# Kernel optimization log

Hardware: AMD Instinct MI355X
Metric: run time of the kernel (lower is better)

## Reference

```python
import jax, jax.numpy as jnp
import numpy as np

EPS = 216.0 / 24389.0
KAPPA = 24389.0 / 27.0
WP = jnp.array([0.95047, 1.0, 1.08883], dtype=jnp.float32)  # D65 white point
M_RGB2XYZ = jnp.array([[0.4124564, 0.3575761, 0.1804375],
                       [0.2126729, 0.7151522, 0.0721750],
                       [0.0193339, 0.1191920, 0.9503041]], dtype=jnp.float32)
M_XYZ2RGB = jnp.array([[3.2404542, -1.5371385, -0.4985314],
                       [-0.9692660, 1.8760108, 0.0415560],
                       [0.0556434, -0.2040259, 1.0572252]], dtype=jnp.float32)
GRID = 8          # cv2.createCLAHE tileGridSize=(8,8)
CLIP_LIMIT = 2.0  # cv2.createCLAHE clipLimit=2.0
NBINS = 256


def _srgb_to_linear(c):
    return jnp.where(c <= 0.04045, c / 12.92, ((c + 0.055) / 1.055) ** 2.4)


def _linear_to_srgb(c):
    c = jnp.maximum(c, 0.0)
    return jnp.where(c <= 0.0031308, c * 12.92, 1.055 * c ** (1.0 / 2.4) - 0.055)


def _rgb_to_lab(rgb):  # rgb [...,3] in [0,1]
    xyz = _srgb_to_linear(rgb) @ M_RGB2XYZ.T / WP
    f = jnp.where(xyz > EPS, jnp.cbrt(xyz), (KAPPA * xyz + 16.0) / 116.0)
    L = 116.0 * f[..., 1] - 16.0
    a = 500.0 * (f[..., 0] - f[..., 1])
    b = 200.0 * (f[..., 1] - f[..., 2])
    return L, a, b


def _lab_to_rgb(L, a, b):
    fy = (L + 16.0) / 116.0
    fx = fy + a / 500.0
    fz = fy - b / 200.0
    def finv(f):
        f3 = f ** 3
        return jnp.where(f3 > EPS, f3, (116.0 * f - 16.0) / KAPPA)
    xyz = jnp.stack([finv(fx), finv(fy), finv(fz)], axis=-1) * WP
    return jnp.clip(_linear_to_srgb(xyz @ M_XYZ2RGB.T), 0.0, 1.0)


def _quantize_L(L):  # cv2.normalize(..., 0, 255, NORM_MINMAX) per image + uint8 cast
    lmin = L.min(axis=(1, 2), keepdims=True)
    lmax = L.max(axis=(1, 2), keepdims=True)
    l255 = (L - lmin) / (lmax - lmin + 1e-6) * 255.0
    return jnp.clip(jnp.round(l255), 0, 255).astype(jnp.int32)


def _equalize_hist(l_int):  # cv2.equalizeHist per image, [N,H,W] int32 -> float levels
    N, H, W = l_int.shape
    seg = (jnp.arange(N, dtype=jnp.int32)[:, None, None] * NBINS + l_int).reshape(-1)
    hist = jax.ops.segment_sum(jnp.ones(seg.shape, jnp.float32), seg,
                               num_segments=N * NBINS).reshape(N, NBINS)
    lut = jnp.round(jnp.cumsum(hist, axis=1) * (255.0 / (H * W)))  # [N,256]
    return jnp.take_along_axis(lut, l_int.reshape(N, H * W), axis=1).reshape(N, H, W)


def _clahe(l_int):  # tiled clipped histogram equalization + bilinear LUT blend
    N, H, W = l_int.shape
    th, tw = H // GRID, W // GRID
    area = th * tw
    ty = jnp.arange(H, dtype=jnp.int32) // th
    tx = jnp.arange(W, dtype=jnp.int32) // tw
    tile = ty[:, None] * GRID + tx[None, :]                      # [H,W] tile id
    seg = ((jnp.arange(N, dtype=jnp.int32)[:, None, None] * (GRID * GRID) + tile)
           * NBINS + l_int).reshape(-1)
    hist = jax.ops.segment_sum(jnp.ones(seg.shape, jnp.float32), seg,
                               num_segments=N * GRID * GRID * NBINS
                               ).reshape(N, GRID, GRID, NBINS)
    limit = max(CLIP_LIMIT * area / NBINS, 1.0)                  # = 32 for 64x64 tiles
    clipped = jnp.minimum(hist, limit)
    excess = (hist - clipped).sum(axis=-1, keepdims=True)
    luts = jnp.round(jnp.cumsum(clipped + excess / NBINS, axis=-1) * (255.0 / area))
    # bilinear interpolation between the 4 neighbouring tile LUTs (border-clamped)
    cy = jnp.clip((jnp.arange(H, dtype=jnp.float32) + 0.5) / th - 0.5, 0.0, GRID - 1.0)
    cx = jnp.clip((jnp.arange(W, dtype=jnp.float32) + 0.5) / tw - 0.5, 0.0, GRID - 1.0)
    y0 = jnp.clip(jnp.floor(cy).astype(jnp.int32), 0, GRID - 2); y1 = y0 + 1
    x0 = jnp.clip(jnp.floor(cx).astype(jnp.int32), 0, GRID - 2); x1 = x0 + 1
    wy = (cy - y0)[:, None]
    wx = (cx - x0)[None, :]
    def per_image(lut, v):  # lut [GRID,GRID,256], v [H,W]
        v00 = lut[y0[:, None], x0[None, :], v]
        v01 = lut[y0[:, None], x1[None, :], v]
        v10 = lut[y1[:, None], x0[None, :], v]
        v11 = lut[y1[:, None], x1[None, :], v]
        top = v00 * (1.0 - wx) + v01 * wx
        bot = v10 * (1.0 - wx) + v11 * wx
        return top * (1.0 - wy) + bot * wy
    return jax.vmap(per_image)(luts, l_int)


def setup_inputs() -> dict:
    key = jax.random.key(0)
    x = jax.random.uniform(key, (16, 3, 512, 512), dtype=jnp.float32)
    return {"x": x}


def reference(x):
    rgb = jnp.transpose(x, (0, 2, 3, 1))          # NCHW -> NHWC
    L, a, b = _rgb_to_lab(rgb)
    l_int = _quantize_L(L)
    def recon(l255):
        out = _lab_to_rgb(l255 * (100.0 / 255.0), a, b)
        return jnp.transpose(out, (0, 3, 1, 2)) * 255.0  # uint8-valued like original
    return recon(_equalize_hist(l_int)), recon(_clahe(l_int))
```

## Files before the change

kernel.cpp:

```cpp
#include <hip/hip_runtime.h>

#define NIMG 16
#define HH 512
#define WW 512
#define HW (HH * WW)
#define NHW (NIMG * HW)
#define TILE 64
#define TILE_AREA (TILE * TILE)

#define EPSV ((float)(216.0 / 24389.0))
#define KAPV ((float)(24389.0 / 27.0))


__device__ __forceinline__ float pow24(float t) {
    float l   = __builtin_amdgcn_logf(t);
    float r   = __builtin_amdgcn_exp2f(l);
    float dl  = (t - r) * __builtin_amdgcn_rcpf(r) * 1.4426950408889634f;
    float ehi = 2.4f * l;
    float elo = __builtin_fmaf(2.4f, l, -ehi) + 2.4f * dl;
    float p   = __builtin_amdgcn_exp2f(ehi);
    return __builtin_fmaf(p * 0.6931471805599453f, elo, p);
}

__device__ __forceinline__ float cbrt_p(float v) {
    float l  = __builtin_amdgcn_logf(v);
    float t  = __builtin_amdgcn_exp2f(l * (1.0f / 3.0f));
    float t2 = t * t;
    float num = __builtin_fmaf(-t2, t, v);
    return __builtin_fmaf(num, __builtin_amdgcn_rcpf(3.0f * t2), t);
}

__device__ __forceinline__ float srgb2lin_p(float c) {
    float lin = c / 12.92f;
    float t   = (c + 0.055f) / 1.055f;
    return (c <= 0.04045f) ? lin : pow24(t);
}

__device__ __forceinline__ float fwd_p(float v) {
    return (v > EPSV) ? cbrt_p(v) : (KAPV * v + 16.0f) / 116.0f;
}

__device__ __forceinline__ float lin2srgb_f(float c) {
    c = fmaxf(c, 0.0f);
    float lo = c * 12.92f;
    float p  = __builtin_amdgcn_exp2f(__builtin_amdgcn_logf(c) * (float)(1.0 / 2.4));
    float hi = 1.055f * p - 0.055f;
    float r  = (c <= 0.0031308f) ? lo : hi;
    return fminf(fmaxf(r, 0.0f), 1.0f);
}

__device__ __forceinline__ float finv_f(float f) {
    float f3 = f * f * f;
    return (f3 > EPSV) ? f3 : (116.0f * f - 16.0f) * (float)(27.0 / 24389.0);
}

__device__ __forceinline__ void lab2rgb255_f(float L, float a, float b,
                                             float* R, float* G, float* B) {
    float fy = (L + 16.0f) * (float)(1.0 / 116.0);
    float fx = fy + a * (float)(1.0 / 500.0);
    float fz = fy - b * (float)(1.0 / 200.0);
    float X = finv_f(fx) * 0.95047f;
    float Y = finv_f(fy);
    float Z = finv_f(fz) * 1.08883f;
    *R = lin2srgb_f((float)3.2404542 * X + (float)-1.5371385 * Y + (float)-0.4985314 * Z) * 255.0f;
    *G = lin2srgb_f((float)-0.969266 * X + (float)1.8760108  * Y + (float)0.041556   * Z) * 255.0f;
    *B = lin2srgb_f((float)0.0556434 * X + (float)-0.2040259 * Y + (float)1.0572252  * Z) * 255.0f;
}

__global__ void k1_lab(const float* __restrict__ x, float* __restrict__ Lbuf,
                       float* __restrict__ out, float* __restrict__ tmn,
                       float* __restrict__ tmx) {
    int n = blockIdx.y, tile = blockIdx.x;
    int b = (n << 6) + tile;
    int ty = tile >> 3, tx = tile & 7;
    int t = threadIdx.x;
    const float* img = x + (size_t)n * 3 * HW;
    float* Lp = Lbuf + (size_t)n * HW;
    float* o0 = out + (size_t)n * 3 * HW;

    float mn = 1e30f, mx = -1e30f;
    #pragma unroll
    for (int it = 0; it < 4; it++) {
        int j = it * 1024 + t * 4;
        int r = j >> 6, c = j & 63;
        int p = (ty * TILE + r) * WW + tx * TILE + c;
        float4 r4 = *(const float4*)(img + p);
        float4 g4 = *(const float4*)(img + HW + p);
        float4 b4 = *(const float4*)(img + 2 * HW + p);
        float4 L4, A4, B4;
        #pragma unroll
        for (int k = 0; k < 4; k++) {
            float rr = ((const float*)&r4)[k];
            float gg = ((const float*)&g4)[k];
            float bb = ((const float*)&b4)[k];
            float rl = srgb2lin_p(rr), gl = srgb2lin_p(gg), bl = srgb2lin_p(bb);
            float X = ((float)0.4124564 * rl + (float)0.3575761 * gl + (float)0.1804375 * bl) / (float)0.95047;
            float Y = ((float)0.2126729 * rl + (float)0.7151522 * gl + (float)0.072175  * bl);
            float Z = ((float)0.0193339 * rl + (float)0.119192  * gl + (float)0.9503041 * bl) / (float)1.08883;
            float fx = fwd_p(X), fy = fwd_p(Y), fz = fwd_p(Z);
            float L = 116.0f * fy - 16.0f;
            ((float*)&L4)[k] = L;
            ((float*)&A4)[k] = 500.0f * (fx - fy);
            ((float*)&B4)[k] = 200.0f * (fy - fz);
            mn = fminf(mn, L);
            mx = fmaxf(mx, L);
        }
        *(float4*)(Lp + p)          = L4;
        *(float4*)(o0 + HW + p)     = A4;
        *(float4*)(o0 + 2 * HW + p) = B4;
    }
    for (int off = 32; off; off >>= 1) {
        mn = fminf(mn, __shfl_down(mn, off, 64));
        mx = fmaxf(mx, __shfl_down(mx, off, 64));
    }
    __shared__ float smn[4], smx[4];
    int wv = t >> 6, ln = t & 63;
    if (ln == 0) { smn[wv] = mn; smx[wv] = mx; }
    __syncthreads();
    if (t == 0) {
        tmn[b] = fminf(fminf(smn[0], smn[1]), fminf(smn[2], smn[3]));
        tmx[b] = fmaxf(fmaxf(smx[0], smx[1]), fmaxf(smx[2], smx[3]));
    }
}

__global__ void k2_quant(const float* __restrict__ Lbuf, const float* __restrict__ tmn,
                         const float* __restrict__ tmx, unsigned char* __restrict__ li_arr,
                         int* __restrict__ hist_tile, float* __restrict__ lut_tile) {
    int n = blockIdx.y, tile = blockIdx.x;
    int b = (n << 6) + tile;
    int ty = tile >> 3, tx = tile & 7;
    int t = threadIdx.x;

    __shared__ int sh[256];
    __shared__ float sred2[2];
    __shared__ int wsum[4];

    if (t < 64) {
        float v = tmn[(n << 6) + t];
        for (int off = 32; off; off >>= 1) v = fminf(v, __shfl_down(v, off, 64));
        if (t == 0) sred2[0] = v;
    } else if (t < 128) {
        float v = tmx[(n << 6) + (t - 64)];
        for (int off = 32; off; off >>= 1) v = fmaxf(v, __shfl_down(v, off, 64));
        if (t == 64) sred2[1] = v;
    }
    sh[t] = 0;
    __syncthreads();
    float lmin = sred2[0], lmax = sred2[1];
    float d = lmax - lmin + (float)1e-6;

    const float* Lp = Lbuf + (size_t)n * HW;
    unsigned char* lio = li_arr + (size_t)n * HW;
    #pragma unroll
    for (int it = 0; it < 4; it++) {
        int j = it * 1024 + t * 4;
        int r = j >> 6, c = j & 63;
        int p = (ty * TILE + r) * WW + tx * TILE + c;
        float4 L4 = *(const float4*)(Lp + p);
        uchar4 li4;
        #pragma unroll
        for (int k = 0; k < 4; k++) {
            float l255 = (((const float*)&L4)[k] - lmin) / d * 255.0f;
            int li = (int)rintf(l255);
            li = min(max(li, 0), 255);
            ((unsigned char*)&li4)[k] = (unsigned char)li;
            atomicAdd(&sh[li], 1);
        }
        *(uchar4*)(lio + p) = li4;
    }
    __syncthreads();
    int h = sh[t];
    hist_tile[b * 256 + t] = h;

    int cl = min(h, 32);
    int sum = cl;
    for (int off = 32; off; off >>= 1) sum += __shfl_down(sum, off, 64);
    int wv = t >> 6, ln = t & 63;
    if (ln == 0) wsum[wv] = sum;
    __syncthreads();
    int total = wsum[0] + wsum[1] + wsum[2] + wsum[3];
    int exc = TILE_AREA - total;
    sh[t] = 256 * cl + exc;
    __syncthreads();
    for (int off = 1; off < 256; off <<= 1) {
        int v = sh[t];
        int add = (t >= off) ? sh[t - off] : 0;
        __syncthreads();
        sh[t] = v + add;
        __syncthreads();
    }
    lut_tile[b * 256 + t] = rintf((float)sh[t] * (float)(255.0 / 1048576.0));
}

__global__ void k3_recon(const unsigned char* __restrict__ li_arr,
                         const int* __restrict__ hist_tile,
                         const float* __restrict__ lut_tile,
                         float* out) {
    int n = blockIdx.y, tile = blockIdx.x;
    int ty = tile >> 3, tx = tile & 7;
    int t = threadIdx.x;

    __shared__ int   sscan[256];
    __shared__ float seq[256];
    __shared__ float slut[9 * 256];

    const int* ht = hist_tile + n * 64 * 256;
    int h2 = 0;
    for (int tile2 = 0; tile2 < 64; tile2++) h2 += ht[tile2 * 256 + t];
    sscan[t] = h2;
    __syncthreads();
    for (int off = 1; off < 256; off <<= 1) {
        int v = sscan[t];
        int add = (t >= off) ? sscan[t - off] : 0;
        __syncthreads();
        sscan[t] = v + add;
        __syncthreads();
    }
    seq[t] = rintf((float)sscan[t] * (float)(255.0 / (double)HW));

    const float* lt = lut_tile + n * 64 * 256;
    for (int j = t; j < 9 * 256; j += 256) {
        int q = j >> 8;
        int jy = q / 3, jx = q % 3;
        int gy = min(max(ty - 1 + jy, 0), 7);
        int gx = min(max(tx - 1 + jx, 0), 7);
        slut[j] = lt[(gy * 8 + gx) * 256 + (j & 255)];
    }
    __syncthreads();

    const unsigned char* lip = li_arr + (size_t)n * HW;
    float* o0 = out + (size_t)n * 3 * HW;
    float* o1 = out + (size_t)3 * NHW + (size_t)n * 3 * HW;

    #pragma unroll
    for (int it = 0; it < 4; it++) {
        int j = it * 1024 + t * 4;
        int r = j >> 6, c = j & 63;
        int y = ty * TILE + r;
        int xb = tx * TILE + c;
        int p = y * WW + xb;

        uchar4 li4 = *(const uchar4*)(lip + p);
        float4 a4 = *(const float4*)(o0 + HW + p);
        float4 b4 = *(const float4*)(o0 + 2 * HW + p);

        float cyf = fminf(fmaxf(((float)y + 0.5f) / 64.0f - 0.5f, 0.0f), 7.0f);
        int y0 = min((int)cyf, 6);
        float wy = cyf - (float)y0;
        int ly = y0 - ty + 1;

        float4 R0, G0, B0, R1, G1, B1;
        #pragma unroll
        for (int k = 0; k < 4; k++) {
            int li = ((const unsigned char*)&li4)[k];
            float A  = ((const float*)&a4)[k];
            float B2 = ((const float*)&b4)[k];
            float l_eq = seq[li];

            int xc = xb + k;
            float cxf = fminf(fmaxf(((float)xc + 0.5f) / 64.0f - 0.5f, 0.0f), 7.0f);
            int x0 = min((int)cxf, 6);
            float wx = cxf - (float)x0;
            int lx = x0 - tx + 1;
            int base = ((ly * 3 + lx) << 8) + li;
            float v00 = slut[base];
            float v01 = slut[base + 256];
            float v10 = slut[base + 768];
            float v11 = slut[base + 1024];
            float top = v00 * (1.0f - wx) + v01 * wx;
            float bot = v10 * (1.0f - wx) + v11 * wx;
            float l_cl = top * (1.0f - wy) + bot * wy;

            float R, G, B;
            lab2rgb255_f(l_eq * (float)(100.0 / 255.0), A, B2, &R, &G, &B);
            ((float*)&R0)[k] = R; ((float*)&G0)[k] = G; ((float*)&B0)[k] = B;
            lab2rgb255_f(l_cl * (float)(100.0 / 255.0), A, B2, &R, &G, &B);
            ((float*)&R1)[k] = R; ((float*)&G1)[k] = G; ((float*)&B1)[k] = B;
        }
        *(float4*)(o0 + p)          = R0;
        *(float4*)(o0 + HW + p)     = G0;
        *(float4*)(o0 + 2 * HW + p) = B0;
        *(float4*)(o1 + p)          = R1;
        *(float4*)(o1 + HW + p)     = G1;
        *(float4*)(o1 + 2 * HW + p) = B1;
    }
}

extern "C" void kernel_launch(void* const* d_in, const int* in_sizes, int n_in,
                              void* d_out, int out_size, void* d_ws, size_t ws_size,
                              hipStream_t stream) {
    const float* x = (const float*)d_in[0];
    float* out = (float*)d_out;
    char* ws = (char*)d_ws;

    float* Lbuf = (float*)ws;
    size_t off = (size_t)NHW * 4;
    unsigned char* li = (unsigned char*)(ws + off); off += NHW;
    int* hist_tile = (int*)(ws + off);    off += (size_t)NIMG * 64 * 256 * 4;
    float* lut_tile = (float*)(ws + off); off += (size_t)NIMG * 64 * 256 * 4;
    float* tmn = (float*)(ws + off);      off += 1024 * 4;
    float* tmx = (float*)(ws + off);      off += 1024 * 4;

    dim3 grid(64, NIMG);
    k1_lab<<<grid, 256, 0, stream>>>(x, Lbuf, out, tmn, tmx);
    k2_quant<<<grid, 256, 0, stream>>>(Lbuf, tmn, tmx, li, hist_tile, lut_tile);
    k3_recon<<<grid, 256, 0, stream>>>(li, hist_tile, lut_tile, out);
}
```

Before: 172.1 us.

## Fuse three kernels into one persistent kernel with grid barriers and register-held Lab

Merges the Lab conversion, quantization/histogram and reconstruction kernels into one kernel that keeps L, a and b values in registers across two software grid barriers. It removes the global round trips for the L buffer, the a/b planes and the quantized byte array. Per-tile histograms are also replaced by atomic accumulation into a per-image histogram. The kernel depends on all 1024 blocks being co-resident, which launch_bounds(256,4) is meant to allow; if they are not, the spin-wait barrier can deadlock. Register pressure also rises from holding 48 floats per thread.

```diff
diff --git a/kernel.cpp b/kernel.cpp
--- a/kernel.cpp
+++ b/kernel.cpp
@@ -7,6 +7,7 @@
 #define NHW (NIMG * HW)
 #define TILE 64
 #define TILE_AREA (TILE * TILE)
+#define NBLOCKS (64 * NIMG)
 
 #define EPSV ((float)(216.0 / 24389.0))
 #define KAPV ((float)(24389.0 / 27.0))
@@ -67,16 +68,55 @@
     *B = lin2srgb_f((float)0.0556434 * X + (float)-0.2040259 * Y + (float)1.0572252  * Z) * 255.0f;
 }
 
-__global__ void k1_lab(const float* __restrict__ x, float* __restrict__ Lbuf,
-                       float* __restrict__ out, float* __restrict__ tmn,
-                       float* __restrict__ tmx) {
-    int n = blockIdx.y, tile = blockIdx.x;
-    int b = (n << 6) + tile;
-    int ty = tile >> 3, tx = tile & 7;
+__device__ __forceinline__ void rst_f(float* p, float v) {
+    __hip_atomic_store(p, v, __ATOMIC_RELAXED, __HIP_MEMORY_SCOPE_AGENT);
+}
+__device__ __forceinline__ float rld_f(const float* p) {
+    return __hip_atomic_load(p, __ATOMIC_RELAXED, __HIP_MEMORY_SCOPE_AGENT);
+}
+__device__ __forceinline__ int rld_i(const int* p) {
+    return __hip_atomic_load(p, __ATOMIC_RELAXED, __HIP_MEMORY_SCOPE_AGENT);
+}
+
+__device__ __forceinline__ void grid_barrier(int* ctr) {
+    __threadfence();
+    __syncthreads();
+    if (threadIdx.x == 0) {
+        __hip_atomic_fetch_add(ctr, 1, __ATOMIC_ACQ_REL, __HIP_MEMORY_SCOPE_AGENT);
+        while (__hip_atomic_load(ctr, __ATOMIC_ACQUIRE, __HIP_MEMORY_SCOPE_AGENT)
+               < NBLOCKS) {
+            __builtin_amdgcn_s_sleep(4);
+        }
+    }
+    __syncthreads();
+}
+
+__global__ void k0_init(int* __restrict__ hist_img, int* __restrict__ ctr) {
     int t = threadIdx.x;
+    if (t < 2) ctr[t] = 0;
+    for (int j = t; j < NIMG * 256; j += 256) hist_img[j] = 0;
+}
+
+__global__ __launch_bounds__(256, 4)
+void k_fused(const float* __restrict__ x, float* __restrict__ out,
+             float* __restrict__ tmn, float* __restrict__ tmx,
+             int* __restrict__ hist_img, float* __restrict__ lut_tile,
+             int* __restrict__ ctr) {
+    const int n = blockIdx.y, tile = blockIdx.x;
+    const int b = (n << 6) + tile;
+    const int ty = tile >> 3, tx = tile & 7;
+    const int t = threadIdx.x;
+
+    __shared__ int   sh[256];
+    __shared__ float smn[4], smx[4];
+    __shared__ float sred2[2];
+    __shared__ int   wsum[4];
+    __shared__ float seq[256];
+    __shared__ float slut[9 * 256];
+
+    float Lr[16], Ar[16], Brr[16];
+
     const float* img = x + (size_t)n * 3 * HW;
-    float* Lp = Lbuf + (size_t)n * HW;
-    float* o0 = out + (size_t)n * 3 * HW;
 
     float mn = 1e30f, mx = -1e30f;
     #pragma unroll
@@ -87,7 +127,6 @@
         float4 r4 = *(const float4*)(img + p);
         float4 g4 = *(const float4*)(img + HW + p);
         float4 b4 = *(const float4*)(img + 2 * HW + p);
-        float4 L4, A4, B4;
         #pragma unroll
         for (int k = 0; k < 4; k++) {
             float rr = ((const float*)&r4)[k];
@@ -99,48 +138,33 @@
             float Z = ((float)0.0193339 * rl + (float)0.119192  * gl + (float)0.9503041 * bl) / (float)1.08883;
             float fx = fwd_p(X), fy = fwd_p(Y), fz = fwd_p(Z);
             float L = 116.0f * fy - 16.0f;
-            ((float*)&L4)[k] = L;
-            ((float*)&A4)[k] = 500.0f * (fx - fy);
-            ((float*)&B4)[k] = 200.0f * (fy - fz);
+            Lr[it * 4 + k]  = L;
+            Ar[it * 4 + k]  = 500.0f * (fx - fy);
+            Brr[it * 4 + k] = 200.0f * (fy - fz);
             mn = fminf(mn, L);
             mx = fmaxf(mx, L);
         }
-        *(float4*)(Lp + p)          = L4;
-        *(float4*)(o0 + HW + p)     = A4;
-        *(float4*)(o0 + 2 * HW + p) = B4;
     }
     for (int off = 32; off; off >>= 1) {
         mn = fminf(mn, __shfl_down(mn, off, 64));
         mx = fmaxf(mx, __shfl_down(mx, off, 64));
     }
-    __shared__ float smn[4], smx[4];
-    int wv = t >> 6, ln = t & 63;
+    const int wv = t >> 6, ln = t & 63;
     if (ln == 0) { smn[wv] = mn; smx[wv] = mx; }
     __syncthreads();
     if (t == 0) {
-        tmn[b] = fminf(fminf(smn[0], smn[1]), fminf(smn[2], smn[3]));
-        tmx[b] = fmaxf(fmaxf(smx[0], smx[1]), fmaxf(smx[2], smx[3]));
-    }
-}
-
-__global__ void k2_quant(const float* __restrict__ Lbuf, const float* __restrict__ tmn,
-                         const float* __restrict__ tmx, unsigned char* __restrict__ li_arr,
-                         int* __restrict__ hist_tile, float* __restrict__ lut_tile) {
-    int n = blockIdx.y, tile = blockIdx.x;
-    int b = (n << 6) + tile;
-    int ty = tile >> 3, tx = tile & 7;
-    int t = threadIdx.x;
-
-    __shared__ int sh[256];
-    __shared__ float sred2[2];
-    __shared__ int wsum[4];
+        rst_f(&tmn[b], fminf(fminf(smn[0], smn[1]), fminf(smn[2], smn[3])));
+        rst_f(&tmx[b], fmaxf(fmaxf(smx[0], smx[1]), fmaxf(smx[2], smx[3])));
+    }
+
+    grid_barrier(&ctr[0]);
 
     if (t < 64) {
-        float v = tmn[(n << 6) + t];
+        float v = rld_f(&tmn[(n << 6) + t]);
         for (int off = 32; off; off >>= 1) v = fminf(v, __shfl_down(v, off, 64));
         if (t == 0) sred2[0] = v;
     } else if (t < 128) {
-        float v = tmx[(n << 6) + (t - 64)];
+        float v = rld_f(&tmx[(n << 6) + (t - 64)]);
         for (int off = 32; off; off >>= 1) v = fmaxf(v, __shfl_down(v, off, 64));
         if (t == 64) sred2[1] = v;
     }
@@ -149,33 +173,28 @@
     float lmin = sred2[0], lmax = sred2[1];
     float d = lmax - lmin + (float)1e-6;
 
-    const float* Lp = Lbuf + (size_t)n * HW;
-    unsigned char* lio = li_arr + (size_t)n * HW;
+    unsigned int lipk[4];
     #pragma unroll
     for (int it = 0; it < 4; it++) {
-        int j = it * 1024 + t * 4;
-        int r = j >> 6, c = j & 63;
-        int p = (ty * TILE + r) * WW + tx * TILE + c;
-        float4 L4 = *(const float4*)(Lp + p);
-        uchar4 li4;
+        unsigned int pk = 0;
         #pragma unroll
         for (int k = 0; k < 4; k++) {
-            float l255 = (((const float*)&L4)[k] - lmin) / d * 255.0f;
+            float l255 = (Lr[it * 4 + k] - lmin) / d * 255.0f;
             int li = (int)rintf(l255);
             li = min(max(li, 0), 255);
-            ((unsigned char*)&li4)[k] = (unsigned char)li;
+            pk |= (unsigned int)li << (8 * k);
             atomicAdd(&sh[li], 1);
         }
-        *(uchar4*)(lio + p) = li4;
+        lipk[it] = pk;
     }
     __syncthreads();
     int h = sh[t];
-    hist_tile[b * 256 + t] = h;
+    __hip_atomic_fetch_add(&hist_img[(n << 8) + t], h,
+                           __ATOMIC_RELAXED, __HIP_MEMORY_SCOPE_AGENT);
 
     int cl = min(h, 32);
     int sum = cl;
     for (int off = 32; off; off >>= 1) sum += __shfl_down(sum, off, 64);
-    int wv = t >> 6, ln = t & 63;
     if (ln == 0) wsum[wv] = sum;
     __syncthreads();
     int total = wsum[0] + wsum[1] + wsum[2] + wsum[3];
@@ -189,34 +208,20 @@
         sh[t] = v + add;
         __syncthreads();
     }
-    lut_tile[b * 256 + t] = rintf((float)sh[t] * (float)(255.0 / 1048576.0));
-}
-
-__global__ void k3_recon(const unsigned char* __restrict__ li_arr,
-                         const int* __restrict__ hist_tile,
-                         const float* __restrict__ lut_tile,
-                         float* out) {
-    int n = blockIdx.y, tile = blockIdx.x;
-    int ty = tile >> 3, tx = tile & 7;
-    int t = threadIdx.x;
-
-    __shared__ int   sscan[256];
-    __shared__ float seq[256];
-    __shared__ float slut[9 * 256];
-
-    const int* ht = hist_tile + n * 64 * 256;
-    int h2 = 0;
-    for (int tile2 = 0; tile2 < 64; tile2++) h2 += ht[tile2 * 256 + t];
-    sscan[t] = h2;
+    rst_f(&lut_tile[b * 256 + t], rintf((float)sh[t] * (float)(255.0 / 1048576.0)));
+
+    grid_barrier(&ctr[1]);
+
+    sh[t] = rld_i(&hist_img[(n << 8) + t]);
     __syncthreads();
     for (int off = 1; off < 256; off <<= 1) {
-        int v = sscan[t];
-        int add = (t >= off) ? sscan[t - off] : 0;
+        int v = sh[t];
+        int add = (t >= off) ? sh[t - off] : 0;
         __syncthreads();
-        sscan[t] = v + add;
+        sh[t] = v + add;
         __syncthreads();
     }
-    seq[t] = rintf((float)sscan[t] * (float)(255.0 / (double)HW));
+    seq[t] = rintf((float)sh[t] * (float)(255.0 / (double)HW));
 
     const float* lt = lut_tile + n * 64 * 256;
     for (int j = t; j < 9 * 256; j += 256) {
@@ -224,11 +229,10 @@
         int jy = q / 3, jx = q % 3;
         int gy = min(max(ty - 1 + jy, 0), 7);
         int gx = min(max(tx - 1 + jx, 0), 7);
-        slut[j] = lt[(gy * 8 + gx) * 256 + (j & 255)];
-    }
-    __syncthreads();
-
-    const unsigned char* lip = li_arr + (size_t)n * HW;
+        slut[j] = rld_f(&lt[(gy * 8 + gx) * 256 + (j & 255)]);
+    }
+    __syncthreads();
+
     float* o0 = out + (size_t)n * 3 * HW;
     float* o1 = out + (size_t)3 * NHW + (size_t)n * 3 * HW;
 
@@ -240,10 +244,6 @@
         int xb = tx * TILE + c;
         int p = y * WW + xb;
 
-        uchar4 li4 = *(const uchar4*)(lip + p);
-        float4 a4 = *(const float4*)(o0 + HW + p);
-        float4 b4 = *(const float4*)(o0 + 2 * HW + p);
-
         float cyf = fminf(fmaxf(((float)y + 0.5f) / 64.0f - 0.5f, 0.0f), 7.0f);
         int y0 = min((int)cyf, 6);
         float wy = cyf - (float)y0;
@@ -252,9 +252,9 @@
         float4 R0, G0, B0, R1, G1, B1;
         #pragma unroll
         for (int k = 0; k < 4; k++) {
-            int li = ((const unsigned char*)&li4)[k];
-            float A  = ((const float*)&a4)[k];
-            float B2 = ((const float*)&b4)[k];
+            int li = (int)((lipk[it] >> (8 * k)) & 255u);
+            float A  = Ar[it * 4 + k];
+            float B2 = Brr[it * 4 + k];
             float l_eq = seq[li];
 
             int xc = xb + k;
@@ -293,16 +293,13 @@
     float* out = (float*)d_out;
     char* ws = (char*)d_ws;
 
-    float* Lbuf = (float*)ws;
-    size_t off = (size_t)NHW * 4;
-    unsigned char* li = (unsigned char*)(ws + off); off += NHW;
-    int* hist_tile = (int*)(ws + off);    off += (size_t)NIMG * 64 * 256 * 4;
-    float* lut_tile = (float*)(ws + off); off += (size_t)NIMG * 64 * 256 * 4;
-    float* tmn = (float*)(ws + off);      off += 1024 * 4;
-    float* tmx = (float*)(ws + off);      off += 1024 * 4;
-
-    dim3 grid(64, NIMG);
-    k1_lab<<<grid, 256, 0, stream>>>(x, Lbuf, out, tmn, tmx);
-    k2_quant<<<grid, 256, 0, stream>>>(Lbuf, tmn, tmx, li, hist_tile, lut_tile);
-    k3_recon<<<grid, 256, 0, stream>>>(li, hist_tile, lut_tile, out);
-}
+    int*   hist_img = (int*)ws;
+    float* lut_tile = (float*)(ws + (size_t)64 * 1024);
+    float* tmn = (float*)(ws + (size_t)64 * 1024 + (size_t)NIMG * 64 * 256 * 4);
+    float* tmx = tmn + 1024;
+    int*   ctr = (int*)(tmx + 1024);
+
+    dim3 grid(64, NIMG), block(256);
+    k0_init<<<1, 256, 0, stream>>>(hist_img, ctr);
+    k_fused<<<grid, block, 0, stream>>>(x, out, tmn, tmx, hist_img, lut_tile, ctr);
+}
```

Measured after the change: 421.8 us. 2.45x slower.
